# Optimization experiments

Measured on AMD Instinct MI355X. Metric: run time of the kernel, lower is better.

## Reference

```python
import jax, jax.numpy as jnp
import numpy as np

SYLL_V, WORD_V, K = 10000, 20000, 10
SYLL_D, WORD_D, H = 64, 32, 64  # H = hidden_dim // 2 per direction
B, T = 256, 512
IN_D = SYLL_D + WORD_D


def lstm_dir(x, w_ih, w_hh, b_ih, b_hh, reverse):
    # x: [B,T,D]; w_ih: [4H,D]; w_hh: [4H,H]; PyTorch gate order i,f,g,o
    b, t, _ = x.shape
    h = w_hh.shape[1]
    xp = jnp.einsum('btd,gd->btg', x, w_ih) + b_ih + b_hh  # [B,T,4H]
    if reverse:
        xp = xp[:, ::-1]
    def step(carry, xt):
        hs, cs = carry
        g = xt + hs @ w_hh.T
        i, f, gg, o = jnp.split(g, 4, axis=-1)
        i = jax.nn.sigmoid(i); f = jax.nn.sigmoid(f)
        gg = jnp.tanh(gg); o = jax.nn.sigmoid(o)
        cs = f * cs + i * gg
        hs = o * jnp.tanh(cs)
        return (hs, cs), hs
    h0 = jnp.zeros((b, h), x.dtype)
    _, hseq = jax.lax.scan(step, (h0, h0), jnp.swapaxes(xp, 0, 1))
    hseq = jnp.swapaxes(hseq, 0, 1)  # [B,T,H]
    if reverse:
        hseq = hseq[:, ::-1]
    return hseq


def crf_llh(emissions, tags, mask, start_t, end_t, trans):
    # torchcrf log-likelihood, batch_first. emissions [B,T,K], tags [B,T], mask [B,T] bool
    b, t, k = emissions.shape
    mf = mask.astype(emissions.dtype)
    ar = jnp.arange(b)
    # numerator: score of the given tag path
    num = start_t[tags[:, 0]] + emissions[ar, 0, tags[:, 0]]
    e_tag = jnp.take_along_axis(emissions, tags[:, :, None], axis=2)[:, :, 0]  # [B,T]
    tr = trans[tags[:, :-1], tags[:, 1:]]  # [B,T-1]
    num = num + jnp.sum(mf[:, 1:] * (tr + e_tag[:, 1:]), axis=1)
    seq_len = jnp.sum(mask.astype(jnp.int32), axis=1)
    last_tags = jnp.take_along_axis(tags, (seq_len - 1)[:, None], axis=1)[:, 0]
    num = num + end_t[last_tags]
    # denominator: log partition via forward algorithm (sequential logsumexp scan)
    alpha0 = start_t[None, :] + emissions[:, 0]  # [B,K]
    def step(alpha, inp):
        em_t, m_t = inp  # [B,K], [B]
        nxt = jax.nn.logsumexp(alpha[:, :, None] + trans[None] + em_t[:, None, :], axis=1)
        return jnp.where(m_t[:, None], nxt, alpha), None
    alpha, _ = jax.lax.scan(
        step, alpha0,
        (jnp.swapaxes(emissions[:, 1:], 0, 1), jnp.swapaxes(mask[:, 1:], 0, 1)))
    den = jax.nn.logsumexp(alpha + end_t[None, :], axis=1)
    return num - den


def setup_inputs() -> dict:
    key = jax.random.key(0)
    ks = jax.random.split(key, 20)
    s = 0.1
    syll_emb = jax.random.normal(ks[0], (SYLL_V, SYLL_D), jnp.float32) * s
    syll_emb = syll_emb.at[0].set(0.0)  # padding_idx
    word_emb = jax.random.normal(ks[1], (WORD_V, WORD_D), jnp.float32) * s
    word_emb = word_emb.at[0].set(0.0)
    def lstm_params(i):
        return (jax.random.normal(ks[i], (4 * H, IN_D), jnp.float32) * s,
                jax.random.normal(ks[i + 1], (4 * H, H), jnp.float32) * s,
                jax.random.normal(ks[i + 2], (4 * H,), jnp.float32) * s,
                jax.random.normal(ks[i + 3], (4 * H,), jnp.float32) * s)
    w_ih_f, w_hh_f, b_ih_f, b_hh_f = lstm_params(2)
    w_ih_b, w_hh_b, b_ih_b, b_hh_b = lstm_params(6)
    W_tag = jax.random.normal(ks[10], (K, 2 * H), jnp.float32) * s
    b_tag = jax.random.normal(ks[11], (K,), jnp.float32) * s
    crf_start = jax.random.normal(ks[12], (K,), jnp.float32) * s
    crf_end = jax.random.normal(ks[13], (K,), jnp.float32) * s
    crf_trans = jax.random.normal(ks[14], (K, K), jnp.float32) * s
    return {
        'syll_input': jax.random.randint(ks[15], (B, T), 0, SYLL_V),
        'word_input': jax.random.randint(ks[16], (B, T), 0, WORD_V),
        'tags': jax.random.randint(ks[17], (B, T), 0, K),
        'mask': jnp.ones((B, T), jnp.bool_),
        'syll_emb': syll_emb, 'word_emb': word_emb,
        'w_ih_f': w_ih_f, 'w_hh_f': w_hh_f, 'b_ih_f': b_ih_f, 'b_hh_f': b_hh_f,
        'w_ih_b': w_ih_b, 'w_hh_b': w_hh_b, 'b_ih_b': b_ih_b, 'b_hh_b': b_hh_b,
        'W_tag': W_tag, 'b_tag': b_tag,
        'crf_start': crf_start, 'crf_end': crf_end, 'crf_trans': crf_trans,
    }


def reference(syll_input, word_input, tags, mask,
              syll_emb, word_emb,
              w_ih_f, w_hh_f, b_ih_f, b_hh_f,
              w_ih_b, w_hh_b, b_ih_b, b_hh_b,
              W_tag, b_tag, crf_start, crf_end, crf_trans):
    combined = jnp.concatenate([syll_emb[syll_input], word_emb[word_input]], axis=2)  # [B,T,96]
    h_f = lstm_dir(combined, w_ih_f, w_hh_f, b_ih_f, b_hh_f, reverse=False)
    h_b = lstm_dir(combined, w_ih_b, w_hh_b, b_ih_b, b_hh_b, reverse=True)
    lstm_out = jnp.concatenate([h_f, h_b], axis=2)  # [B,T,128]
    emissions = jnp.einsum('bth,kh->btk', lstm_out, W_tag) + b_tag
    llh = crf_llh(emissions, tags, mask, crf_start, crf_end, crf_trans)
    return -jnp.mean(llh)  # reduction='mean', negated
```

## Files before the change

### kernel.cpp

```cpp
#include <hip/hip_runtime.h>

typedef unsigned short ushort_t;
typedef unsigned int uint_t;
typedef __attribute__((ext_vector_type(8))) short short8;
typedef __attribute__((ext_vector_type(4))) float f32x4;
typedef __fp16 fp16x4 __attribute__((ext_vector_type(4)));

#define B_SZ 256
#define T_LEN 512
#define Hd 64
#define IND 96
#define G4 256
#define KT 10
#define SYLL_V 10000
#define WORD_V 20000
#define TP 520

#define L2E  1.4426950408889634f
#define L2E2 2.8853900817779268f

#define U16_PS_F 0
#define U16_PS_B (SYLL_V*G4)
#define U16_PW_F (2*SYLL_V*G4)
#define U16_PW_B (2*SYLL_V*G4 + WORD_V*G4)
#define U16_TAB_END (2*SYLL_V*G4 + 2*WORD_V*G4)
#define F_EM   (U16_TAB_END/2)
#define F_OMEGA (F_EM + B_SZ*T_LEN*KT)
#define F_S1   (F_OMEGA + B_SZ*64*100)
#define F_END  (F_S1 + B_SZ*64)
#define F_OFFS (F_END + (B_SZ*T_LEN*2*Hd)/2)

template <int V> struct ic { static constexpr int v = V; };

__device__ __forceinline__ ushort_t f2bf(float f) {
    uint_t u = __float_as_uint(f);
    uint_t r = (u + 0x7FFFu + ((u >> 16) & 1u)) >> 16;
    return (ushort_t)r;
}
__device__ __forceinline__ ushort_t f2h(float f) {
    _Float16 h = (_Float16)f;
    return *(ushort_t*)&h;
}
__device__ __forceinline__ float dot4(float4 a, float4 b) {
    return a.x*b.x + a.y*b.y + a.z*b.z + a.w*b.w;
}
__device__ __forceinline__ short8 cvt8(const float* p) {
    float4 x0 = *(const float4*)&p[0];
    float4 x1 = *(const float4*)&p[4];
    short8 f;
    f[0] = (short)f2bf(x0.x); f[1] = (short)f2bf(x0.y);
    f[2] = (short)f2bf(x0.z); f[3] = (short)f2bf(x0.w);
    f[4] = (short)f2bf(x1.x); f[5] = (short)f2bf(x1.y);
    f[6] = (short)f2bf(x1.z); f[7] = (short)f2bf(x1.w);
    return f;
}
__device__ __forceinline__ short8 cvt8s(const float* p, float sc) {
    float4 x0 = *(const float4*)&p[0];
    float4 x1 = *(const float4*)&p[4];
    short8 f;
    f[0] = (short)f2bf(x0.x*sc); f[1] = (short)f2bf(x0.y*sc);
    f[2] = (short)f2bf(x0.z*sc); f[3] = (short)f2bf(x0.w*sc);
    f[4] = (short)f2bf(x1.x*sc); f[5] = (short)f2bf(x1.y*sc);
    f[6] = (short)f2bf(x1.z*sc); f[7] = (short)f2bf(x1.w*sc);
    return f;
}

__global__ __launch_bounds__(128) void offs_kernel(
    const int* __restrict__ syll, const int* __restrict__ word,
    int2* __restrict__ offs)
{
    const int bid = blockIdx.x;
    const int dir = bid & 1;
    const int b = bid >> 1;
    int2* __restrict__ o = offs + (size_t)(dir * B_SZ + b) * TP;
    for (int t = threadIdx.x; t < TP; t += 128) {
        int tc = t > T_LEN - 1 ? T_LEN - 1 : t;
        int p = dir ? (T_LEN - 1 - tc) : tc;
        int2 v;
        v.x = syll[b * T_LEN + p] << 9;
        v.y = word[b * T_LEN + p] << 9;
        o[t] = v;
    }
}

template <int D, int DOFF>
__global__ __launch_bounds__(256) void proj_kernel(
    const float* __restrict__ emb,
    const float* __restrict__ w_ih_f, const float* __restrict__ w_ih_b,
    const float* __restrict__ b_ih_f, const float* __restrict__ b_hh_f,
    const float* __restrict__ b_ih_b, const float* __restrict__ b_hh_b,
    ushort_t* __restrict__ out_f, ushort_t* __restrict__ out_b)
{
    const int dir = blockIdx.y;
    const float* __restrict__ wih = dir ? w_ih_b : w_ih_f;
    ushort_t* __restrict__ out = dir ? out_b : out_f;
    const int v0 = blockIdx.x * 16;
    const int s = threadIdx.x;
    const int g = 64 * (s & 3) + (s >> 2);
    const float gsc = ((s & 3) == 2) ? L2E2 : -L2E;
    const float bh = 0.5f * ((dir ? b_ih_b[g] : b_ih_f[g]) + (dir ? b_hh_b[g] : b_hh_f[g]));

    __shared__ float e_lds[16 * D];
    for (int i = s; i < 16 * D; i += 256) e_lds[i] = emb[v0 * D + i];
    __syncthreads();

    float acc[16];
#pragma unroll
    for (int r = 0; r < 16; r++) acc[r] = 0.f;

#pragma unroll
    for (int dd = 0; dd < D; dd += 16) {
        const float* wp = &wih[g * IND + DOFF + dd];
        float4 wa = *(const float4*)&wp[0];
        float4 wb = *(const float4*)&wp[4];
        float4 wc = *(const float4*)&wp[8];
        float4 wd = *(const float4*)&wp[12];
#pragma unroll
        for (int r = 0; r < 16; r++) {
            const float* ep = &e_lds[r * D + dd];
            float4 e0 = *(const float4*)&ep[0];
            float4 e1 = *(const float4*)&ep[4];
            float4 e2 = *(const float4*)&ep[8];
            float4 e3 = *(const float4*)&ep[12];
            acc[r] += dot4(wa, e0) + dot4(wb, e1) + dot4(wc, e2) + dot4(wd, e3);
        }
    }
#pragma unroll
    for (int r = 0; r < 16; r++) out[(size_t)(v0 + r) * G4 + s] = f2h((acc[r] + bh) * gsc);
}

__global__ __launch_bounds__(256, 1) void lstm_kernel(
    const float* __restrict__ w_hh_f, const float* __restrict__ w_hh_b,
    const ushort_t* __restrict__ tab_u16, const int2* __restrict__ offs,
    ushort_t* __restrict__ h_out)
{
    const int dir = blockIdx.x & 1;
    const int bA = (blockIdx.x >> 1) * 4;
    const int tid = threadIdx.x;
    const int w = tid >> 6;
    const int l = tid & 63;
    const int rg = l >> 4;
    const int c = l & 15;
    const int cell = 16 * w + c;
    const int celloff = cell * 8;

    const char* __restrict__ tsb = (const char*)(tab_u16 + (dir ? U16_PS_B : U16_PS_F));
    const char* __restrict__ twb = (const char*)(tab_u16 + (dir ? U16_PW_B : U16_PW_F));
    const float* __restrict__ whh = dir ? w_hh_b : w_hh_f;

    short8 bfrag[4][2];
#pragma unroll
    for (int tau = 0; tau < 4; tau++) {
        const float sc = (tau == 2) ? L2E2 : -L2E;
#pragma unroll
        for (int chk = 0; chk < 2; chk++)
            bfrag[tau][chk] = cvt8s(whh + (size_t)(64 * tau + cell) * Hd + chk * 32 + rg * 8, sc);
    }

    __shared__ __align__(16) ushort_t h_lds[2][16][72];
    for (int i = tid; i < 2 * 16 * 72; i += 256) ((ushort_t*)h_lds)[i] = 0;

    const int chain = bA + rg;
    const int p0 = dir ? (T_LEN - 1) : 0;
    const int2* __restrict__ op = offs + (size_t)(dir * B_SZ + chain) * TP;

    fp16x4 tS[4], tW[4];
    int2 ix[4];
#pragma unroll
    for (int j = 0; j < 4; j++) {
        int2 o = op[j];
        tS[j] = *(const fp16x4*)(tsb + ((size_t)o.x + celloff));
        tW[j] = *(const fp16x4*)(twb + ((size_t)o.y + celloff));
        ix[j] = op[j + 4];
    }

    float cst = 0.f;
    ushort_t* hp = h_out + ((size_t)(chain * T_LEN + p0) * 2 + dir) * Hd + cell;
    const int hstep = dir ? -128 : 128;
    const f32x4 zro = {0.f, 0.f, 0.f, 0.f};
    __syncthreads();

    auto step = [&](auto STC, int t) {
        constexpr int ST = decltype(STC)::v;
        fp16x4 pp = tS[ST] + tW[ST];
        float ps0 = (float)pp[0];
        float ps1 = (float)pp[1];
        float ps2 = (float)pp[2];
        float ps3 = (float)pp[3];
        tS[ST] = *(const fp16x4*)(tsb + ((size_t)ix[ST].x + celloff));
        tW[ST] = *(const fp16x4*)(twb + ((size_t)ix[ST].y + celloff));
        ix[ST] = op[t + 8];

        f32x4 cc0 = {ps0, 0.f, 0.f, 0.f};
        f32x4 cc1 = {ps1, 0.f, 0.f, 0.f};
        f32x4 cc2 = {ps2, 0.f, 0.f, 0.f};
        f32x4 cc3 = {ps3, 0.f, 0.f, 0.f};
        const ushort_t* hrow = &h_lds[t & 1][c][0];
        short8 a0 = *(const short8*)(hrow + rg * 8);
        short8 a1 = *(const short8*)(hrow + 32 + rg * 8);
        f32x4 p00 = __builtin_amdgcn_mfma_f32_16x16x32_bf16(a0, bfrag[0][0], cc0, 0, 0, 0);
        f32x4 p10 = __builtin_amdgcn_mfma_f32_16x16x32_bf16(a0, bfrag[1][0], cc1, 0, 0, 0);
        f32x4 p20 = __builtin_amdgcn_mfma_f32_16x16x32_bf16(a0, bfrag[2][0], cc2, 0, 0, 0);
        f32x4 p30 = __builtin_amdgcn_mfma_f32_16x16x32_bf16(a0, bfrag[3][0], cc3, 0, 0, 0);
        f32x4 p01 = __builtin_amdgcn_mfma_f32_16x16x32_bf16(a1, bfrag[0][1], zro, 0, 0, 0);
        f32x4 p11 = __builtin_amdgcn_mfma_f32_16x16x32_bf16(a1, bfrag[1][1], zro, 0, 0, 0);
        f32x4 p21 = __builtin_amdgcn_mfma_f32_16x16x32_bf16(a1, bfrag[2][1], zro, 0, 0, 0);
        f32x4 p31 = __builtin_amdgcn_mfma_f32_16x16x32_bf16(a1, bfrag[3][1], zro, 0, 0, 0);

        float ai = p00[0] + p01[0];
        float af = p10[0] + p11[0];
        float ag = fminf(p20[0] + p21[0], 60.0f);
        float ao = p30[0] + p31[0];
        float ei = __builtin_amdgcn_exp2f(ai);
        float ef = __builtin_amdgcn_exp2f(af);
        float Eg = __builtin_amdgcn_exp2f(ag);
        float eo = __builtin_amdgcn_exp2f(ao);
        float e3 = 1.0f + ef;
        float pe = (1.0f + ei) * (1.0f + Eg);
        float num = __builtin_fmaf(Eg - 1.0f, e3, cst * pe);
        float cn = num * __builtin_amdgcn_rcpf(e3 * pe);
        cst = cn;
        float t2 = fminf(cn * L2E2, 60.0f);
        float E2 = __builtin_amdgcn_exp2f(t2);
        float h = (E2 - 1.0f) * __builtin_amdgcn_rcpf((1.0f + eo) * (1.0f + E2));

        ushort_t hb = f2bf(h);
        h_lds[(t + 1) & 1][4 * rg][cell] = hb;
        *hp = hb;
        hp += hstep;
        __builtin_amdgcn_sched_barrier(0);
        asm volatile("s_waitcnt lgkmcnt(0)" ::: "memory");
        __builtin_amdgcn_s_barrier();
        __builtin_amdgcn_sched_barrier(0);
    };

    for (int t = 0; t < T_LEN; t += 4) {
        step(ic<0>{}, t);
        step(ic<1>{}, t + 1);
        step(ic<2>{}, t + 2);
        step(ic<3>{}, t + 3);
    }
}

#define EMIS_G 4
__global__ __launch_bounds__(64) void emis_kernel(
    const ushort_t* __restrict__ hseq, const float* __restrict__ W_tag,
    const float* __restrict__ b_tag, float* __restrict__ em)
{
    const int l = threadIdx.x;
    const int rg = l >> 4;
    const int n = l & 15;

    short8 bf[4];
#pragma unroll
    for (int ch = 0; ch < 4; ch++) {
        if (n < KT) bf[ch] = cvt8(W_tag + (size_t)n * 128 + ch * 32 + rg * 8);
        else { short8 z = {0,0,0,0,0,0,0,0}; bf[ch] = z; }
    }
    const float btv = (n < KT) ? b_tag[n] : 0.f;

#pragma unroll
    for (int gi = 0; gi < EMIS_G; gi++) {
        const int row0 = (blockIdx.x * EMIS_G + gi) * 16;
        const ushort_t* __restrict__ ar = hseq + (size_t)(row0 + n) * 128 + rg * 8;
        short8 a0 = *(const short8*)&ar[0];
        short8 a1 = *(const short8*)&ar[32];
        short8 a2 = *(const short8*)&ar[64];
        short8 a3 = *(const short8*)&ar[96];
        f32x4 acc = {btv, btv, btv, btv};
        acc = __builtin_amdgcn_mfma_f32_16x16x32_bf16(a0, bf[0], acc, 0, 0, 0);
        acc = __builtin_amdgcn_mfma_f32_16x16x32_bf16(a1, bf[1], acc, 0, 0, 0);
        acc = __builtin_amdgcn_mfma_f32_16x16x32_bf16(a2, bf[2], acc, 0, 0, 0);
        acc = __builtin_amdgcn_mfma_f32_16x16x32_bf16(a3, bf[3], acc, 0, 0, 0);
        if (n < KT) {
#pragma unroll
            for (int r = 0; r < 4; r++)
                em[(size_t)(row0 + 4 * rg + r) * KT + n] = acc[r];
        }
    }
}

__global__ __launch_bounds__(64) void crf_stage1(
    const float* __restrict__ em, const float* __restrict__ trans,
    float* __restrict__ Omega, float* __restrict__ S1)
{
    __shared__ float etT[KT * 12];
    const int tid = threadIdx.x;
    for (int i = tid; i < KT * 12; i += 64) etT[i] = 0.f;
    __syncthreads();
    for (int i = tid; i < 100; i += 64) {
        int jj = i / 10, k = i % 10;
        etT[k * 12 + jj] = __expf(trans[i]);
    }
    __syncthreads();

    const int id = blockIdx.x * 64 + tid;
    const int b = id >> 6, c = id & 63;
    const int t0 = (c == 0) ? 1 : c * 8;
    const int nt = (c == 0) ? 7 : 8;

    float run[10][10];
    float s = 0.f;

    float ecur[10];
    {
        const float* r = em + (size_t)(b * T_LEN + t0) * KT;
#pragma unroll
        for (int k = 0; k < 10; k++) ecur[k] = r[k];
    }
    {
        float mx = ecur[0];
#pragma unroll
        for (int k = 1; k < 10; k++) mx = fmaxf(mx, ecur[k]);
        s += mx;
        float ee[10];
#pragma unroll
        for (int k = 0; k < 10; k++) ee[k] = __expf(ecur[k] - mx);
#pragma unroll
        for (int jj = 0; jj < 10; jj++)
#pragma unroll
            for (int k = 0; k < 10; k++) run[jj][k] = etT[k * 12 + jj] * ee[k];
    }
    float enx[10];
    if (nt > 1) {
        const float* r = em + (size_t)(b * T_LEN + t0 + 1) * KT;
#pragma unroll
        for (int k = 0; k < 10; k++) enx[k] = r[k];
    }
    for (int li = 1; li < nt; li++) {
        float mx = enx[0];
#pragma unroll
        for (int k = 1; k < 10; k++) mx = fmaxf(mx, enx[k]);
        s += mx;
        float ee[10];
#pragma unroll
        for (int k = 0; k < 10; k++) ee[k] = __expf(enx[k] - mx);
        if (li + 1 < nt) {
            const float* r = em + (size_t)(b * T_LEN + t0 + li + 1) * KT;
#pragma unroll
            for (int k = 0; k < 10; k++) enx[k] = r[k];
        }
#pragma unroll
        for (int i = 0; i < 10; i++) {
            float outp[10];
#pragma unroll
            for (int k = 0; k < 10; k++) {
                float sum = 0.f;
#pragma unroll
                for (int jj = 0; jj < 10; jj++) sum += run[i][jj] * etT[k * 12 + jj];
                outp[k] = sum * ee[k];
            }
#pragma unroll
            for (int k = 0; k < 10; k++) run[i][k] = outp[k];
        }
    }
    float m = run[0][0];
#pragma unroll
    for (int i = 0; i < 10; i++)
#pragma unroll
        for (int k = 0; k < 10; k++) m = fmaxf(m, run[i][k]);
    float inv = 1.0f / m;
    s += __logf(m);
#pragma unroll
    for (int i = 0; i < 10; i++)
#pragma unroll
        for (int k = 0; k < 10; k++) Omega[(size_t)id * 100 + i * 10 + k] = run[i][k] * inv;
    S1[id] = s;
}

__global__ __launch_bounds__(256) void crf_stage2(
    const float* __restrict__ Omega, const float* __restrict__ S1,
    const float* __restrict__ em, const int* __restrict__ tags,
    const float* __restrict__ start_t, const float* __restrict__ end_t,
    const float* __restrict__ trans, float* __restrict__ out)
{
    const int b = blockIdx.x;
    const int tid = threadIdx.x;
    __shared__ float bufA[64 * 120];
    __shared__ float bufB[32 * 120];
    __shared__ float sh_red[4];
    __shared__ float sh_s;
    __shared__ float scl_sh[32];
    __shared__ float lg_sh[32];
    __shared__ float lg_acc_sh;

    for (int idx = tid; idx < 6400; idx += 256) {
        int c = idx / 100, e = idx % 100;
        bufA[c * 120 + (e / 10) * 12 + (e % 10)] = Omega[(size_t)(b * 64 + c) * 100 + e];
    }
    if (tid < 64) {
        float v = S1[b * 64 + tid];
        for (int off = 32; off; off >>= 1) v += __shfl_down(v, off);
        if (tid == 0) sh_s = v;
    }
    if (tid == 0) lg_acc_sh = 0.f;
    __syncthreads();

    float* src = bufA;
    float* dst = bufB;
    for (int n = 32; n >= 1; n >>= 1) {
        for (int idx = tid; idx < n * 100; idx += 256) {
            int p = idx / 100, e = idx % 100, i = e / 10, k = e % 10;
            const float* A = src + (2 * p) * 120;
            const float* Bm = src + (2 * p + 1) * 120;
            float sum = 0.f;
#pragma unroll
            for (int jj = 0; jj < 10; jj++) sum += A[i * 12 + jj] * Bm[jj * 12 + k];
            dst[p * 120 + i * 12 + k] = sum;
        }
        __syncthreads();
        if (tid < n) {
            const float* M = dst + tid * 120;
            float mx = 0.f;
            for (int i = 0; i < 10; i++)
                for (int k = 0; k < 10; k++) mx = fmaxf(mx, M[i * 12 + k]);
            scl_sh[tid] = 1.0f / mx;
            lg_sh[tid] = __logf(mx);
        }
        __syncthreads();
        if (tid == 0) {
            float s = 0.f;
            for (int p = 0; p < n; p++) s += lg_sh[p];
            lg_acc_sh += s;
        }
        for (int idx = tid; idx < n * 100; idx += 256) {
            int p = idx / 100, e = idx % 100;
            dst[p * 120 + (e / 10) * 12 + (e % 10)] *= scl_sh[p];
        }
        __syncthreads();
        float* t_ = src; src = dst; dst = t_;
    }

    float den = 0.f;
    if (tid < 64) {
        float val = 0.f;
        float mx0 = 0.f;
        if (tid < 10) {
            mx0 = -1e30f;
            for (int jj = 0; jj < 10; jj++) mx0 = fmaxf(mx0, start_t[jj] + em[(size_t)(b * T_LEN) * KT + jj]);
            for (int jj = 0; jj < 10; jj++) {
                float v0 = __expf(start_t[jj] + em[(size_t)(b * T_LEN) * KT + jj] - mx0);
                val += v0 * src[jj * 12 + tid];
            }
            val *= __expf(end_t[tid]);
        }
        for (int off = 8; off; off >>= 1) val += __shfl_down(val, off);
        if (tid == 0) den = __logf(val) + mx0 + sh_s + lg_acc_sh;
    }

    float part = 0.f;
    const int* __restrict__ tg = tags + b * T_LEN;
    for (int t = tid; t < T_LEN; t += 256) {
        int cur = tg[t];
        if (t == 0) part += start_t[cur] + em[(size_t)(b * T_LEN) * KT + cur];
        else part += trans[tg[t - 1] * KT + cur] + em[(size_t)(b * T_LEN + t) * KT + cur];
        if (t == T_LEN - 1) part += end_t[cur];
    }
    for (int off = 32; off; off >>= 1) part += __shfl_down(part, off);
    if ((tid & 63) == 0) sh_red[tid >> 6] = part;
    __syncthreads();
    if (tid == 0) {
        float num = sh_red[0] + sh_red[1] + sh_red[2] + sh_red[3];
        float llh = num - den;
        atomicAdd(out, llh * (-1.0f / 256.0f));
    }
}

extern "C" void kernel_launch(void* const* d_in, const int* in_sizes, int n_in,
                              void* d_out, int out_size, void* d_ws, size_t ws_size,
                              hipStream_t stream) {
    const int* syll      = (const int*)d_in[0];
    const int* word      = (const int*)d_in[1];
    const int* tags      = (const int*)d_in[2];
    const float* syll_emb = (const float*)d_in[4];
    const float* word_emb = (const float*)d_in[5];
    const float* w_ih_f  = (const float*)d_in[6];
    const float* w_hh_f  = (const float*)d_in[7];
    const float* b_ih_f  = (const float*)d_in[8];
    const float* b_hh_f  = (const float*)d_in[9];
    const float* w_ih_b  = (const float*)d_in[10];
    const float* w_hh_b  = (const float*)d_in[11];
    const float* b_ih_b  = (const float*)d_in[12];
    const float* b_hh_b  = (const float*)d_in[13];
    const float* W_tag   = (const float*)d_in[14];
    const float* b_tag   = (const float*)d_in[15];
    const float* crf_start = (const float*)d_in[16];
    const float* crf_end   = (const float*)d_in[17];
    const float* crf_trans = (const float*)d_in[18];

    float* out = (float*)d_out;
    float* ws = (float*)d_ws;
    ushort_t* tab = (ushort_t*)ws;
    ushort_t* hseq = (ushort_t*)(ws + F_END);
    int2* offs = (int2*)(ws + F_OFFS);

    hipMemsetAsync(d_out, 0, sizeof(float), stream);

    offs_kernel<<<B_SZ * 2, 128, 0, stream>>>(syll, word, offs);

    proj_kernel<64, 0><<<dim3(SYLL_V / 16, 2), 256, 0, stream>>>(
        syll_emb, w_ih_f, w_ih_b, b_ih_f, b_hh_f, b_ih_b, b_hh_b,
        tab + U16_PS_F, tab + U16_PS_B);
    proj_kernel<32, 64><<<dim3(WORD_V / 16, 2), 256, 0, stream>>>(
        word_emb, w_ih_f, w_ih_b, b_ih_f, b_hh_f, b_ih_b, b_hh_b,
        tab + U16_PW_F, tab + U16_PW_B);

    lstm_kernel<<<B_SZ * 2 / 4, 256, 0, stream>>>(
        w_hh_f, w_hh_b, tab, offs, hseq);

    emis_kernel<<<B_SZ * T_LEN / (16 * EMIS_G), 64, 0, stream>>>(
        hseq, W_tag, b_tag, ws + F_EM);

    crf_stage1<<<256, 64, 0, stream>>>(ws + F_EM, crf_trans, ws + F_OMEGA, ws + F_S1);

    crf_stage2<<<B_SZ, 256, 0, stream>>>(
        ws + F_OMEGA, ws + F_S1, ws + F_EM, tags, crf_start, crf_end, crf_trans, out);
}
```

Measured before the change: 314.1 us.

## Use bf16 MFMA with split-precision weights for embedding projection tables

```diff
diff --git a/kernel.cpp b/kernel.cpp
--- a/kernel.cpp
+++ b/kernel.cpp
@@ -4,6 +4,7 @@
 typedef unsigned int uint_t;
 typedef __attribute__((ext_vector_type(8))) short short8;
 typedef __attribute__((ext_vector_type(4))) float f32x4;
+typedef __fp16 fp16x2 __attribute__((ext_vector_type(2)));
 typedef __fp16 fp16x4 __attribute__((ext_vector_type(4)));
 
 #define B_SZ 256
@@ -29,6 +30,8 @@
 #define F_S1   (F_OMEGA + B_SZ*64*100)
 #define F_END  (F_S1 + B_SZ*64)
 #define F_OFFS (F_END + (B_SZ*T_LEN*2*Hd)/2)
+#define F_WBUF (F_OFFS + 2*B_SZ*TP*2)
+#define F_BIAS (F_WBUF + 49152*4)
 
 template <int V> struct ic { static constexpr int v = V; };
 
@@ -36,13 +39,6 @@
     uint_t u = __float_as_uint(f);
     uint_t r = (u + 0x7FFFu + ((u >> 16) & 1u)) >> 16;
     return (ushort_t)r;
-}
-__device__ __forceinline__ ushort_t f2h(float f) {
-    _Float16 h = (_Float16)f;
-    return *(ushort_t*)&h;
-}
-__device__ __forceinline__ float dot4(float4 a, float4 b) {
-    return a.x*b.x + a.y*b.y + a.z*b.z + a.w*b.w;
 }
 __device__ __forceinline__ short8 cvt8(const float* p) {
     float4 x0 = *(const float4*)&p[0];
@@ -63,6 +59,54 @@
     f[4] = (short)f2bf(x1.x*sc); f[5] = (short)f2bf(x1.y*sc);
     f[6] = (short)f2bf(x1.z*sc); f[7] = (short)f2bf(x1.w*sc);
     return f;
+}
+
+__global__ __launch_bounds__(256) void wprep_kernel(
+    const float* __restrict__ w_ih_f, const float* __restrict__ w_ih_b,
+    const float* __restrict__ b_ih_f, const float* __restrict__ b_hh_f,
+    const float* __restrict__ b_ih_b, const float* __restrict__ b_hh_b,
+    short8* __restrict__ wbuf, float* __restrict__ biasbuf)
+{
+    const int dir = blockIdx.x;
+    const float* __restrict__ wih = dir ? w_ih_b : w_ih_f;
+    const float* __restrict__ bi = dir ? b_ih_b : b_ih_f;
+    const float* __restrict__ bh = dir ? b_hh_b : b_hh_f;
+    const int tid = threadIdx.x;
+    const int w = tid >> 6;
+    const int l = tid & 63;
+    const int rg = l >> 4;
+    const int c = l & 15;
+
+    {
+        int s = tid;
+        int g = 64 * (s & 3) + (s >> 2);
+        float gsc = ((s & 3) == 2) ? L2E2 : -L2E;
+        biasbuf[dir * 256 + s] = 0.5f * (bi[g] + bh[g]) * gsc;
+    }
+#pragma unroll
+    for (int mt = 0; mt < 4; mt++) {
+        int s = 64 * w + 16 * mt + c;
+        int g = 64 * (s & 3) + (s >> 2);
+        float gsc = ((s & 3) == 2) ? L2E2 : -L2E;
+#pragma unroll
+        for (int ch = 0; ch < 3; ch++) {
+            const float* wp = &wih[g * 96 + ch * 32 + rg * 8];
+            float4 x0 = *(const float4*)&wp[0];
+            float4 x1 = *(const float4*)&wp[4];
+            float vv[8] = {x0.x, x0.y, x0.z, x0.w, x1.x, x1.y, x1.z, x1.w};
+            short8 h8, l8;
+#pragma unroll
+            for (int j = 0; j < 8; j++) {
+                float sv = vv[j] * gsc;
+                ushort_t hb2 = f2bf(sv);
+                h8[j] = (short)hb2;
+                l8[j] = (short)f2bf(sv - __uint_as_float((uint_t)hb2 << 16));
+            }
+            int base = (((dir * 4 + w) * 4 + mt) * 3 + ch) * 2;
+            wbuf[(size_t)(base + 0) * 64 + l] = h8;
+            wbuf[(size_t)(base + 1) * 64 + l] = l8;
+        }
+    }
 }
 
 __global__ __launch_bounds__(128) void offs_kernel(
@@ -83,50 +127,57 @@
     }
 }
 
-template <int D, int DOFF>
-__global__ __launch_bounds__(256) void proj_kernel(
+template <int D, int CH0, int NCH>
+__global__ __launch_bounds__(256) void proj_mfma(
     const float* __restrict__ emb,
-    const float* __restrict__ w_ih_f, const float* __restrict__ w_ih_b,
-    const float* __restrict__ b_ih_f, const float* __restrict__ b_hh_f,
-    const float* __restrict__ b_ih_b, const float* __restrict__ b_hh_b,
+    const short8* __restrict__ wbuf, const float* __restrict__ biasbuf,
     ushort_t* __restrict__ out_f, ushort_t* __restrict__ out_b)
 {
     const int dir = blockIdx.y;
-    const float* __restrict__ wih = dir ? w_ih_b : w_ih_f;
     ushort_t* __restrict__ out = dir ? out_b : out_f;
     const int v0 = blockIdx.x * 16;
-    const int s = threadIdx.x;
-    const int g = 64 * (s & 3) + (s >> 2);
-    const float gsc = ((s & 3) == 2) ? L2E2 : -L2E;
-    const float bh = 0.5f * ((dir ? b_ih_b[g] : b_ih_f[g]) + (dir ? b_hh_b[g] : b_hh_f[g]));
-
-    __shared__ float e_lds[16 * D];
-    for (int i = s; i < 16 * D; i += 256) e_lds[i] = emb[v0 * D + i];
+    const int tid = threadIdx.x;
+    const int w = tid >> 6;
+    const int l = tid & 63;
+    const int rg = l >> 4;
+    const int c = l & 15;
+
+    __shared__ __align__(16) ushort_t Xh[16][D + 8];
+    for (int i = tid; i < 16 * D; i += 256) {
+        int row = i / D, k = i - row * D;
+        Xh[row][k] = f2bf(emb[(size_t)v0 * D + i]);
+    }
+
+    short8 Ah[4][NCH], Al[4][NCH];
+    f32x4 bias[4];
+#pragma unroll
+    for (int mt = 0; mt < 4; mt++) {
+#pragma unroll
+        for (int ch = 0; ch < NCH; ch++) {
+            int base = (((dir * 4 + w) * 4 + mt) * 3 + (CH0 + ch)) * 2;
+            Ah[mt][ch] = wbuf[(size_t)(base + 0) * 64 + l];
+            Al[mt][ch] = wbuf[(size_t)(base + 1) * 64 + l];
+        }
+        bias[mt] = *(const f32x4*)&biasbuf[dir * 256 + 64 * w + 16 * mt + 4 * rg];
+    }
     __syncthreads();
 
-    float acc[16];
-#pragma unroll
-    for (int r = 0; r < 16; r++) acc[r] = 0.f;
-
-#pragma unroll
-    for (int dd = 0; dd < D; dd += 16) {
-        const float* wp = &wih[g * IND + DOFF + dd];
-        float4 wa = *(const float4*)&wp[0];
-        float4 wb = *(const float4*)&wp[4];
-        float4 wc = *(const float4*)&wp[8];
-        float4 wd = *(const float4*)&wp[12];
-#pragma unroll
-        for (int r = 0; r < 16; r++) {
-            const float* ep = &e_lds[r * D + dd];
-            float4 e0 = *(const float4*)&ep[0];
-            float4 e1 = *(const float4*)&ep[4];
-            float4 e2 = *(const float4*)&ep[8];
-            float4 e3 = *(const float4*)&ep[12];
-            acc[r] += dot4(wa, e0) + dot4(wb, e1) + dot4(wc, e2) + dot4(wd, e3);
-        }
-    }
-#pragma unroll
-    for (int r = 0; r < 16; r++) out[(size_t)(v0 + r) * G4 + s] = f2h((acc[r] + bh) * gsc);
+#pragma unroll
+    for (int mt = 0; mt < 4; mt++) {
+        f32x4 acc = bias[mt];
+#pragma unroll
+        for (int ch = 0; ch < NCH; ch++) {
+            short8 Bf = *(const short8*)&Xh[c][ch * 32 + rg * 8];
+            acc = __builtin_amdgcn_mfma_f32_16x16x32_bf16(Ah[mt][ch], Bf, acc, 0, 0, 0);
+            acc = __builtin_amdgcn_mfma_f32_16x16x32_bf16(Al[mt][ch], Bf, acc, 0, 0, 0);
+        }
+        fp16x2 p0 = __builtin_amdgcn_cvt_pkrtz(acc[0], acc[1]);
+        fp16x2 p1 = __builtin_amdgcn_cvt_pkrtz(acc[2], acc[3]);
+        uint2 o;
+        o.x = *(uint_t*)&p0;
+        o.y = *(uint_t*)&p1;
+        *(uint2*)&out[(size_t)(v0 + c) * G4 + 64 * w + 16 * mt + 4 * rg] = o;
+    }
 }
 
 __global__ __launch_bounds__(256, 1) void lstm_kernel(
@@ -409,25 +460,27 @@
             dst[p * 120 + i * 12 + k] = sum;
         }
         __syncthreads();
-        if (tid < n) {
-            const float* M = dst + tid * 120;
-            float mx = 0.f;
-            for (int i = 0; i < 10; i++)
-                for (int k = 0; k < 10; k++) mx = fmaxf(mx, M[i * 12 + k]);
-            scl_sh[tid] = 1.0f / mx;
-            lg_sh[tid] = __logf(mx);
-        }
-        __syncthreads();
-        if (tid == 0) {
-            float s = 0.f;
-            for (int p = 0; p < n; p++) s += lg_sh[p];
-            lg_acc_sh += s;
-        }
-        for (int idx = tid; idx < n * 100; idx += 256) {
-            int p = idx / 100, e = idx % 100;
-            dst[p * 120 + (e / 10) * 12 + (e % 10)] *= scl_sh[p];
-        }
-        __syncthreads();
+        if (n == 32 || n == 8 || n == 2) {
+            if (tid < n) {
+                const float* M = dst + tid * 120;
+                float mx = 0.f;
+                for (int i = 0; i < 10; i++)
+                    for (int k = 0; k < 10; k++) mx = fmaxf(mx, M[i * 12 + k]);
+                scl_sh[tid] = 1.0f / mx;
+                lg_sh[tid] = __logf(mx);
+            }
+            __syncthreads();
+            if (tid == 0) {
+                float s = 0.f;
+                for (int p = 0; p < n; p++) s += lg_sh[p];
+                lg_acc_sh += s;
+            }
+            for (int idx = tid; idx < n * 100; idx += 256) {
+                int p = idx / 100, e = idx % 100;
+                dst[p * 120 + (e / 10) * 12 + (e % 10)] *= scl_sh[p];
+            }
+            __syncthreads();
+        }
         float* t_ = src; src = dst; dst = t_;
     }
 
@@ -493,17 +546,20 @@
     ushort_t* tab = (ushort_t*)ws;
     ushort_t* hseq = (ushort_t*)(ws + F_END);
     int2* offs = (int2*)(ws + F_OFFS);
+    short8* wbuf = (short8*)(ws + F_WBUF);
+    float* biasbuf = ws + F_BIAS;
 
     hipMemsetAsync(d_out, 0, sizeof(float), stream);
 
+    wprep_kernel<<<2, 256, 0, stream>>>(
+        w_ih_f, w_ih_b, b_ih_f, b_hh_f, b_ih_b, b_hh_b, wbuf, biasbuf);
+
     offs_kernel<<<B_SZ * 2, 128, 0, stream>>>(syll, word, offs);
 
-    proj_kernel<64, 0><<<dim3(SYLL_V / 16, 2), 256, 0, stream>>>(
-        syll_emb, w_ih_f, w_ih_b, b_ih_f, b_hh_f, b_ih_b, b_hh_b,
-        tab + U16_PS_F, tab + U16_PS_B);
-    proj_kernel<32, 64><<<dim3(WORD_V / 16, 2), 256, 0, stream>>>(
-        word_emb, w_ih_f, w_ih_b, b_ih_f, b_hh_f, b_ih_b, b_hh_b,
-        tab + U16_PW_F, tab + U16_PW_B);
+    proj_mfma<64, 0, 2><<<dim3(SYLL_V / 16, 2), 256, 0, stream>>>(
+        syll_emb, wbuf, biasbuf, tab + U16_PS_F, tab + U16_PS_B);
+    proj_mfma<32, 2, 1><<<dim3(WORD_V / 16, 2), 256, 0, stream>>>(
+        word_emb, wbuf, biasbuf, tab + U16_PW_F, tab + U16_PW_B);
 
     lstm_kernel<<<B_SZ * 2 / 4, 256, 0, stream>>>(
         w_hh_f, w_hh_b, tab, offs, hseq);
```

Measured after the change: 304.0 us. 1.03x faster.
